# Optimization experiments

Hardware: AMD Instinct MI355X
Metric: run time of the kernel (lower is better)

## Reference

```python
import jax, jax.numpy as jnp
import numpy as np
from jax import lax

K, HE, HD = 4, 96, 192  # kernel_size, hidden_enc, hidden_dec (HD == 2*HE required by z -> decoder hidden)

def _conv1d(x, W, b):
    y = lax.conv_general_dilated(x, W, (1,), 'VALID', dimension_numbers=('NCH', 'OIH', 'NCH'))
    return y + b[None, :, None]

def _maxpool1d(x, k):
    return lax.reduce_window(x, -jnp.inf, lax.max, (1, 1, k), (1, 1, k), 'VALID')

def _gru_scan(x, h0, Wi, Wh, bi, bh, emit):
    # x: (B, S, D); standard PyTorch GRU cell math
    xw = jnp.einsum('bsd,gd->sbg', x, Wi) + bi  # (S, B, 3H)
    def step(h, xw_t):
        xr, xz, xn = jnp.split(xw_t, 3, axis=-1)
        hr, hz, hn = jnp.split(h @ Wh.T + bh, 3, axis=-1)
        r = jax.nn.sigmoid(xr + hr)
        zg = jax.nn.sigmoid(xz + hz)
        n = jnp.tanh(xn + r * hn)
        h_new = (1.0 - zg) * n + zg * h
        return h_new, (h_new if emit else None)
    return lax.scan(step, h0, xw)

def _bigru(x, Wif, Whf, bif, bhf, Wib, Whb, bib, bhb, H):
    h0 = jnp.zeros((x.shape[0], H), x.dtype)
    _, of = _gru_scan(x, h0, Wif, Whf, bif, bhf, True)           # (S, B, H)
    _, ob = _gru_scan(x[:, ::-1], h0, Wib, Whb, bib, bhb, True)  # reverse direction
    return jnp.swapaxes(jnp.concatenate([of, ob[::-1]], axis=-1), 0, 1)  # (B, S, 2H)

def _forward(input, W_c1, b_c1, W_c2, b_c2, Wi_muf, Wh_muf, bi_muf, bh_muf, Wi_mub, Wh_mub, bi_mub, bh_mub, Wi_sgf, Wh_sgf, bi_sgf, bh_sgf, Wi_sgb, Wh_sgb, bi_sgb, bh_sgb, Wi_d, Wh_d, bi_d, bh_d, Wl, bl):
    T = input.shape[1]  # input: (B, T, T); input_dim == seq_len == T
    # Encoder: NodeConv (conv -> relu -> maxpool -> conv -> relu); dropout=0 -> identity
    h = jax.nn.relu(_conv1d(input, W_c1, b_c1))
    h = _maxpool1d(h, K)
    h = jax.nn.relu(_conv1d(h, W_c2, b_c2))  # (B, C, F)
    om = _bigru(h, Wi_muf, Wh_muf, bi_muf, bh_muf, Wi_mub, Wh_mub, bi_mub, bh_mub, HE)
    mu = jnp.concatenate([om[:, -1, :HE], om[:, 0, HE:]], axis=1)
    og = _bigru(h, Wi_sgf, Wh_sgf, bi_sgf, bh_sgf, Wi_sgb, Wh_sgb, bi_sgb, bh_sgb, HE)
    logvar = jnp.concatenate([og[:, -1, :HE], og[:, 0, HE:]], axis=1)
    eps = jax.random.normal(jax.random.key(42), mu.shape, mu.dtype)  # fixed-eps reparameterize
    z = mu + eps * jnp.exp(0.5 * logvar)  # (B, HD)
    # Decoder: leave-one-out per-timestep GRU recompute; hidden carried across outer steps
    base = jnp.arange(T - 1)
    def outer(h_c, i):
        idx = base + (base >= i).astype(base.dtype)  # indices skipping position i
        seq = jnp.take(input, idx, axis=1)           # (B, T-1, T)
        h_new, _ = _gru_scan(seq, h_c, Wi_d, Wh_d, bi_d, bh_d, False)
        return h_new, h_new @ Wl.T + bl
    _, outs = lax.scan(outer, z, jnp.arange(T))
    return jnp.swapaxes(outs, 0, 1), mu, logvar  # (B, T, T), (B, HD), (B, HD)

def setup_inputs():
    keys = iter(jax.random.split(jax.random.key(0), 40))
    def w(*shape):
        return jax.random.normal(next(keys), shape, jnp.float32) * 0.1
    B, D, C, F = 16, 96, 64, 20  # F = ((96-4+1)//4) - 4 + 1
    inp = {"input": jax.random.normal(next(keys), (B, D, D), jnp.float32)}
    inp["W_c1"], inp["b_c1"] = w(C, D, K), jnp.zeros((C,), jnp.float32)
    inp["W_c2"], inp["b_c2"] = w(C, C, K), jnp.zeros((C,), jnp.float32)
    for nm in ["muf", "mub", "sgf", "sgb"]:
        inp["Wi_" + nm] = w(3 * HE, F)
        inp["Wh_" + nm] = w(3 * HE, HE)
        inp["bi_" + nm] = jnp.zeros((3 * HE,), jnp.float32)
        inp["bh_" + nm] = jnp.zeros((3 * HE,), jnp.float32)
    inp["Wi_d"], inp["Wh_d"] = w(3 * HD, D), w(3 * HD, HD)
    inp["bi_d"], inp["bh_d"] = jnp.zeros((3 * HD,), jnp.float32), jnp.zeros((3 * HD,), jnp.float32)
    inp["Wl"], inp["bl"] = w(D, HD), jnp.zeros((D,), jnp.float32)
    return inp

def reference(input, W_c1, b_c1, W_c2, b_c2, Wi_muf, Wh_muf, bi_muf, bh_muf, Wi_mub, Wh_mub, bi_mub, bh_mub, Wi_sgf, Wh_sgf, bi_sgf, bh_sgf, Wi_sgb, Wh_sgb, bi_sgb, bh_sgb, Wi_d, Wh_d, bi_d, bh_d, Wl, bl):
    return _forward(input, W_c1, b_c1, W_c2, b_c2, Wi_muf, Wh_muf, bi_muf, bh_muf, Wi_mub, Wh_mub, bi_mub, bh_mub, Wi_sgf, Wh_sgf, bi_sgf, bh_sgf, Wi_sgb, Wh_sgb, bi_sgb, bh_sgb, Wi_d, Wh_d, bi_d, bh_d, Wl, bl)
```

## Files before the change

kernel.cpp:

```cpp
#include <hip/hip_runtime.h>
#include <math.h>
#include <stdint.h>


namespace {

constexpr int B  = 16;
constexpr int T  = 96;
constexpr int C  = 64;
constexpr int L1 = 93;
constexpr int LP = 23;
constexpr int F  = 20;
constexpr int HE = 96;
constexpr int GE = 288;
constexpr int HD = 192;
constexpr int GD = 576;
constexpr int SD = 95;

constexpr int WS_HENC = 0;
constexpr int WS_Z    = WS_HENC + B * C * F;
constexpr int WS_XW   = WS_Z + B * HD;
constexpr int WS_WHH  = WS_XW + B * T * GD;

constexpr int OUT_MU = B * T * T;
constexpr int OUT_LV = OUT_MU + B * HD;

typedef _Float16 half8 __attribute__((ext_vector_type(8)));
typedef float f32x4  __attribute__((ext_vector_type(4)));

constexpr float LOG2E  = 1.4426950408889634f;
constexpr float LOG2E2 = 2.8853900817779268f;

__device__ __forceinline__ float sigmf(float x) { return 1.0f / (1.0f + expf(-x)); }

__device__ __forceinline__ float fsig(float v) {
  float u = __builtin_amdgcn_exp2f(v * -LOG2E);
  return __builtin_amdgcn_rcpf(1.0f + u);
}
__device__ __forceinline__ float ftanh(float v) {
  float u = __builtin_amdgcn_exp2f(v * LOG2E2);
  return fmaf(-2.0f, __builtin_amdgcn_rcpf(1.0f + u), 1.0f);
}

__global__ __launch_bounds__(256) void enc_conv(
    const float* __restrict__ input, const float* __restrict__ Wc1,
    const float* __restrict__ bc1, const float* __restrict__ Wc2,
    const float* __restrict__ bc2, float* __restrict__ h_enc) {
  __shared__ float xin[T * T];
  __shared__ float y1[C * L1];
  const int b = blockIdx.x;
  for (int i = threadIdx.x; i < T * T; i += 256) xin[i] = input[b * T * T + i];
  __syncthreads();
  for (int idx = threadIdx.x; idx < C * L1; idx += 256) {
    const int o = idx / L1, t = idx - o * L1;
    const float* w = Wc1 + o * (T * 4);
    float acc = bc1[o];
#pragma unroll 8
    for (int i = 0; i < T; ++i) {
      float4 wv = *reinterpret_cast<const float4*>(w + i * 4);
      const float* xp = xin + i * T + t;
      acc = fmaf(wv.x, xp[0], acc);
      acc = fmaf(wv.y, xp[1], acc);
      acc = fmaf(wv.z, xp[2], acc);
      acc = fmaf(wv.w, xp[3], acc);
    }
    y1[idx] = fmaxf(acc, 0.0f);
  }
  __syncthreads();
  float* pl = xin;
  for (int idx = threadIdx.x; idx < C * LP; idx += 256) {
    const int o = idx / LP, t = idx - o * LP;
    const float* yp = y1 + o * L1 + 4 * t;
    pl[idx] = fmaxf(fmaxf(yp[0], yp[1]), fmaxf(yp[2], yp[3]));
  }
  __syncthreads();
  for (int idx = threadIdx.x; idx < C * F; idx += 256) {
    const int o = idx / F, t = idx - o * F;
    const float* w = Wc2 + o * (C * 4);
    float acc = bc2[o];
#pragma unroll 8
    for (int i = 0; i < C; ++i) {
      float4 wv = *reinterpret_cast<const float4*>(w + i * 4);
      const float* xp = pl + i * LP + t;
      acc = fmaf(wv.x, xp[0], acc);
      acc = fmaf(wv.y, xp[1], acc);
      acc = fmaf(wv.z, xp[2], acc);
      acc = fmaf(wv.w, xp[3], acc);
    }
    h_enc[b * (C * F) + idx] = fmaxf(acc, 0.0f);
  }
}

__global__ __launch_bounds__(320) void enc_gru(
    const float* __restrict__ h_enc,
    const float* __restrict__ Wi0, const float* __restrict__ Wh0,
    const float* __restrict__ bi0, const float* __restrict__ bh0,
    const float* __restrict__ Wi1, const float* __restrict__ Wh1,
    const float* __restrict__ bi1, const float* __restrict__ bh1,
    const float* __restrict__ Wi2, const float* __restrict__ Wh2,
    const float* __restrict__ bi2, const float* __restrict__ bh2,
    const float* __restrict__ Wi3, const float* __restrict__ Wh3,
    const float* __restrict__ bi3, const float* __restrict__ bh3,
    float* __restrict__ out) {
  const int chain = blockIdx.x >> 4;
  const int b = blockIdx.x & 15;
  const float *Wi, *Wh, *bi, *bh;
  if (chain == 0)      { Wi = Wi0; Wh = Wh0; bi = bi0; bh = bh0; }
  else if (chain == 1) { Wi = Wi1; Wh = Wh1; bi = bi1; bh = bh1; }
  else if (chain == 2) { Wi = Wi2; Wh = Wh2; bi = bi2; bh = bh2; }
  else                 { Wi = Wi3; Wh = Wh3; bi = bi3; bh = bh3; }
  const bool fwd = (chain & 1) == 0;
  const int off = ((chain >> 1) ? OUT_LV : OUT_MU) + b * HD + (fwd ? 0 : HE);

  __shared__ float xall[C * F];
  __shared__ float h[HE];
  __shared__ float gx[GE], ghs[GE];

  const int tid = threadIdx.x;
  for (int i = tid; i < C * F; i += 320) xall[i] = h_enc[b * (C * F) + i];
  if (tid < HE) h[tid] = 0.0f;

  float wi[F], wh[HE], big = 0.0f, bhg = 0.0f;
  if (tid < GE) {
#pragma unroll
    for (int d = 0; d < F; ++d) wi[d] = Wi[tid * F + d];
#pragma unroll
    for (int k = 0; k < HE; ++k) wh[k] = Wh[tid * HE + k];
    big = bi[tid];
    bhg = bh[tid];
  }
  __syncthreads();

  for (int s = 0; s < C; ++s) {
    const int se = fwd ? s : (C - 1 - s);
    if (tid < GE) {
      const float* xr = xall + se * F;
      float ax = big, ah = bhg;
#pragma unroll
      for (int d = 0; d < F; ++d) ax = fmaf(wi[d], xr[d], ax);
#pragma unroll
      for (int k = 0; k < HE; ++k) ah = fmaf(wh[k], h[k], ah);
      gx[tid] = ax;
      ghs[tid] = ah;
    }
    __syncthreads();
    if (tid < HE) {
      const float r  = sigmf(gx[tid] + ghs[tid]);
      const float zg = sigmf(gx[HE + tid] + ghs[HE + tid]);
      const float n  = tanhf(fmaf(r, ghs[2 * HE + tid], gx[2 * HE + tid]));
      h[tid] = fmaf(zg, h[tid] - n, n);
    }
    __syncthreads();
  }
  if (tid < HE) out[off + tid] = h[tid];
}

__device__ __forceinline__ uint32_t rotl32(uint32_t v, int d) {
  return (v << d) | (v >> (32 - d));
}

__device__ __forceinline__ float erfinv32(float x) {
  float w = -log1pf(-x * x);
  float p;
  if (w < 5.0f) {
    w -= 2.5f;
    p = 2.81022636e-08f;
    p = fmaf(p, w, 3.43273939e-07f);
    p = fmaf(p, w, -3.5233877e-06f);
    p = fmaf(p, w, -4.39150654e-06f);
    p = fmaf(p, w, 0.00021858087f);
    p = fmaf(p, w, -0.00125372503f);
    p = fmaf(p, w, -0.00417768164f);
    p = fmaf(p, w, 0.246640727f);
    p = fmaf(p, w, 1.50140941f);
  } else {
    w = sqrtf(w) - 3.0f;
    p = -0.000200214257f;
    p = fmaf(p, w, 0.000100950558f);
    p = fmaf(p, w, 0.00134934322f);
    p = fmaf(p, w, -0.00367342844f);
    p = fmaf(p, w, 0.00573950773f);
    p = fmaf(p, w, -0.0076224613f);
    p = fmaf(p, w, 0.00943887047f);
    p = fmaf(p, w, 1.00167406f);
    p = fmaf(p, w, 2.83297682f);
  }
  return p * x;
}

__global__ __launch_bounds__(256) void z_kernel(const float* __restrict__ dout,
                                                float* __restrict__ z) {
  const int p = blockIdx.x * 256 + threadIdx.x;
  if (p >= 1536) return;
  const uint32_t ks0 = 0u, ks1 = 42u;
  const uint32_t ks2 = 0x1BD11BDAu ^ ks0 ^ ks1;
  uint32_t x0 = (uint32_t)p + ks0;
  uint32_t x1 = (uint32_t)(p + 1536) + ks1;
  x0 += x1; x1 = rotl32(x1, 13) ^ x0;
  x0 += x1; x1 = rotl32(x1, 15) ^ x0;
  x0 += x1; x1 = rotl32(x1, 26) ^ x0;
  x0 += x1; x1 = rotl32(x1, 6)  ^ x0;
  x0 += ks1; x1 += ks2 + 1u;
  x0 += x1; x1 = rotl32(x1, 17) ^ x0;
  x0 += x1; x1 = rotl32(x1, 29) ^ x0;
  x0 += x1; x1 = rotl32(x1, 16) ^ x0;
  x0 += x1; x1 = rotl32(x1, 24) ^ x0;
  x0 += ks2; x1 += ks0 + 2u;
  x0 += x1; x1 = rotl32(x1, 13) ^ x0;
  x0 += x1; x1 = rotl32(x1, 15) ^ x0;
  x0 += x1; x1 = rotl32(x1, 26) ^ x0;
  x0 += x1; x1 = rotl32(x1, 6)  ^ x0;
  x0 += ks0; x1 += ks1 + 3u;
  x0 += x1; x1 = rotl32(x1, 17) ^ x0;
  x0 += x1; x1 = rotl32(x1, 29) ^ x0;
  x0 += x1; x1 = rotl32(x1, 16) ^ x0;
  x0 += x1; x1 = rotl32(x1, 24) ^ x0;
  x0 += ks1; x1 += ks2 + 4u;
  x0 += x1; x1 = rotl32(x1, 13) ^ x0;
  x0 += x1; x1 = rotl32(x1, 15) ^ x0;
  x0 += x1; x1 = rotl32(x1, 26) ^ x0;
  x0 += x1; x1 = rotl32(x1, 6)  ^ x0;
  x0 += ks2; x1 += ks0 + 5u;

  const float* mu = dout + OUT_MU;
  const float* lv = dout + OUT_LV;
  const float lo = -0.99999994f;
#pragma unroll
  for (int half = 0; half < 2; ++half) {
    const uint32_t bits = half ? x1 : x0;
    const int e = half ? (p + 1536) : p;
    const float f = __builtin_bit_cast(float, (bits >> 9) | 0x3F800000u) - 1.0f;
    const float u = fmaxf(lo, fmaf(f, 2.0f, lo));
    const float eps = 1.41421356f * erfinv32(u);
    z[e] = fmaf(eps, expf(0.5f * lv[e]), mu[e]);
  }
}

__global__ __launch_bounds__(192) void dec_xw(const float* __restrict__ input,
                                              const float* __restrict__ Wi,
                                              const float* __restrict__ bi,
                                              const float* __restrict__ bh,
                                              float* __restrict__ XW) {
  const int br = blockIdx.x;
  __shared__ float xrow[T];
  if (threadIdx.x < T) xrow[threadIdx.x] = input[br * T + threadIdx.x];
  __syncthreads();
  for (int g = threadIdx.x; g < GD; g += 192) {
    const float* w = Wi + g * T;
    float acc = bi[g] + (g < 2 * HD ? bh[g] : 0.0f);
#pragma unroll 8
    for (int d = 0; d < T; ++d) acc = fmaf(w[d], xrow[d], acc);
    XW[br * GD + g] = acc;
  }
}

__global__ __launch_bounds__(256) void wh_to_f16(const float* __restrict__ w,
                                                 _Float16* __restrict__ o) {
  const int i = blockIdx.x * 256 + threadIdx.x;
  if (i < GD * HD) o[i] = (_Float16)w[i];
}

__global__ __launch_bounds__(768) void decoder(
    const float* __restrict__ XW, const _Float16* __restrict__ WhH,
    const float* __restrict__ bh, const float* __restrict__ z,
    const float* __restrict__ Wl, const float* __restrict__ bl,
    float* __restrict__ dout) {
  const int b = blockIdx.x;
  const int tid = threadIdx.x;
  const int lane = tid & 63;
  const int w = tid >> 6;
  const int col = lane & 15;
  const int g4 = lane >> 4;
  const int hidx = 16 * w + col;

  __shared__ alignas(16) _Float16 hb[2][HD];
  __shared__ alignas(16) float hf[HD];

  half8 bR[6], bZ[6], bN[6];
#pragma unroll
  for (int kk = 0; kk < 6; ++kk) {
    const int ko = 32 * kk + 8 * g4;
    bR[kk] = *reinterpret_cast<const half8*>(WhH + hidx * HD + ko);
    bZ[kk] = *reinterpret_cast<const half8*>(WhH + (HD + hidx) * HD + ko);
    bN[kk] = *reinterpret_cast<const half8*>(WhH + (2 * HD + hidx) * HD + ko);
  }
  const float bhn = bh[2 * HD + hidx];

  float hold = z[b * HD + hidx];
  if (g4 == 0) hb[0][hidx] = (_Float16)hold;
  __syncthreads();

  const f32x4 kZero = {0.0f, 0.0f, 0.0f, 0.0f};
  int cur = 0;
  const float* xwb = XW + b * T * GD;

  for (int i = 0; i < T; ++i) {
    for (int s = 0; s < SD; ++s) {
      const int rr = s + (s >= i ? 1 : 0);
      const float* xwrow = xwb + rr * GD;
      const float xr = xwrow[hidx];
      const float xz = xwrow[HD + hidx];
      const float xn = xwrow[2 * HD + hidx];

      half8 a[6];
#pragma unroll
      for (int kk = 0; kk < 6; ++kk)
        a[kk] = *reinterpret_cast<const half8*>(&hb[cur][32 * kk + 8 * g4]);

      f32x4 aR = __builtin_amdgcn_mfma_f32_16x16x32_f16(a[0], bR[0], kZero, 0, 0, 0);
      f32x4 aZ = __builtin_amdgcn_mfma_f32_16x16x32_f16(a[0], bZ[0], kZero, 0, 0, 0);
      f32x4 aN = __builtin_amdgcn_mfma_f32_16x16x32_f16(a[0], bN[0], kZero, 0, 0, 0);
#pragma unroll
      for (int kk = 1; kk < 6; ++kk) {
        aR = __builtin_amdgcn_mfma_f32_16x16x32_f16(a[kk], bR[kk], aR, 0, 0, 0);
        aZ = __builtin_amdgcn_mfma_f32_16x16x32_f16(a[kk], bZ[kk], aZ, 0, 0, 0);
        aN = __builtin_amdgcn_mfma_f32_16x16x32_f16(a[kk], bN[kk], aN, 0, 0, 0);
      }
      const float r  = fsig(xr + aR[0]);
      const float zg = fsig(xz + aZ[0]);
      const float n  = ftanh(fmaf(r, aN[0] + bhn, xn));
      hold = fmaf(zg, hold - n, n);

      if (g4 == 0) {
        hb[cur ^ 1][hidx] = (_Float16)hold;
        if (s == SD - 1) hf[hidx] = hold;
      }
      __syncthreads();
      cur ^= 1;
    }
    if (tid < T) {
      const float4* wl = reinterpret_cast<const float4*>(Wl + tid * HD);
      const float4* hv = reinterpret_cast<const float4*>(hf);
      float a0 = bl[tid], a1 = 0.f, a2 = 0.f, a3 = 0.f;
#pragma unroll
      for (int k = 0; k < HD / 4; k += 4) {
        float4 w0 = wl[k], h0 = hv[k];
        float4 w1 = wl[k + 1], h1 = hv[k + 1];
        float4 w2 = wl[k + 2], h2 = hv[k + 2];
        float4 w3 = wl[k + 3], h3 = hv[k + 3];
        a0 = fmaf(w0.x, h0.x, fmaf(w0.y, h0.y, fmaf(w0.z, h0.z, fmaf(w0.w, h0.w, a0))));
        a1 = fmaf(w1.x, h1.x, fmaf(w1.y, h1.y, fmaf(w1.z, h1.z, fmaf(w1.w, h1.w, a1))));
        a2 = fmaf(w2.x, h2.x, fmaf(w2.y, h2.y, fmaf(w2.z, h2.z, fmaf(w2.w, h2.w, a2))));
        a3 = fmaf(w3.x, h3.x, fmaf(w3.y, h3.y, fmaf(w3.z, h3.z, fmaf(w3.w, h3.w, a3))));
      }
      dout[(b * T + i) * T + tid] = (a0 + a1) + (a2 + a3);
    }
  }
}

}

extern "C" void kernel_launch(void* const* d_in, const int* in_sizes, int n_in,
                              void* d_out, int out_size, void* d_ws,
                              size_t ws_size, hipStream_t stream) {
  const float* input  = (const float*)d_in[0];
  const float* Wc1    = (const float*)d_in[1];
  const float* bc1    = (const float*)d_in[2];
  const float* Wc2    = (const float*)d_in[3];
  const float* bc2    = (const float*)d_in[4];
  const float* Wi_muf = (const float*)d_in[5];
  const float* Wh_muf = (const float*)d_in[6];
  const float* bi_muf = (const float*)d_in[7];
  const float* bh_muf = (const float*)d_in[8];
  const float* Wi_mub = (const float*)d_in[9];
  const float* Wh_mub = (const float*)d_in[10];
  const float* bi_mub = (const float*)d_in[11];
  const float* bh_mub = (const float*)d_in[12];
  const float* Wi_sgf = (const float*)d_in[13];
  const float* Wh_sgf = (const float*)d_in[14];
  const float* bi_sgf = (const float*)d_in[15];
  const float* bh_sgf = (const float*)d_in[16];
  const float* Wi_sgb = (const float*)d_in[17];
  const float* Wh_sgb = (const float*)d_in[18];
  const float* bi_sgb = (const float*)d_in[19];
  const float* bh_sgb = (const float*)d_in[20];
  const float* Wi_d   = (const float*)d_in[21];
  const float* Wh_d   = (const float*)d_in[22];
  const float* bi_d   = (const float*)d_in[23];
  const float* bh_d   = (const float*)d_in[24];
  const float* Wl     = (const float*)d_in[25];
  const float* bl     = (const float*)d_in[26];

  float* ws = (float*)d_ws;
  float* h_enc = ws + WS_HENC;
  float* zbuf  = ws + WS_Z;
  float* XW    = ws + WS_XW;
  _Float16* WhH = (_Float16*)(ws + WS_WHH);
  float* out = (float*)d_out;

  enc_conv<<<B, 256, 0, stream>>>(input, Wc1, bc1, Wc2, bc2, h_enc);
  enc_gru<<<64, 320, 0, stream>>>(h_enc, Wi_muf, Wh_muf, bi_muf, bh_muf,
                                  Wi_mub, Wh_mub, bi_mub, bh_mub,
                                  Wi_sgf, Wh_sgf, bi_sgf, bh_sgf,
                                  Wi_sgb, Wh_sgb, bi_sgb, bh_sgb, out);
  z_kernel<<<6, 256, 0, stream>>>(out, zbuf);
  dec_xw<<<B * T, 192, 0, stream>>>(input, Wi_d, bi_d, bh_d, XW);
  wh_to_f16<<<(GD * HD + 255) / 256, 256, 0, stream>>>(Wh_d, WhH);
  decoder<<<B, 768, 0, stream>>>(XW, WhH, bh_d, zbuf, Wl, bl, out);
}
```

Before: 6.453 ms.

## Batch all decoder sequences into the MFMA M dimension in one block

The decoder now runs as a single 768-thread block that puts all 16 batch rows into the M dimension of each 16x16x32 MFMA. Previously each of 16 blocks used only row 0 of its MFMA output, so most of every tile was wasted. Each lane now handles four batch rows per step: it loads their XW gate inputs and does the gate math for each. LOG2E factors are folded into XW, the f16 recurrent weights and the bias, which removes the scaling multiplies from the sigmoid and tanh paths, and the shared hidden buffers are padded to a stride of 200. The cost is more per-step work on the serial critical path inside one CU, while the other CUs sit idle.

```diff
diff --git a/kernel.cpp b/kernel.cpp
--- a/kernel.cpp
+++ b/kernel.cpp
@@ -16,6 +16,7 @@
 constexpr int HD = 192;
 constexpr int GD = 576;
 constexpr int SD = 95;
+constexpr int HS = 200;
 
 constexpr int WS_HENC = 0;
 constexpr int WS_Z    = WS_HENC + B * C * F;
@@ -33,13 +34,11 @@
 
 __device__ __forceinline__ float sigmf(float x) { return 1.0f / (1.0f + expf(-x)); }
 
-__device__ __forceinline__ float fsig(float v) {
-  float u = __builtin_amdgcn_exp2f(v * -LOG2E);
-  return __builtin_amdgcn_rcpf(1.0f + u);
-}
-__device__ __forceinline__ float ftanh(float v) {
-  float u = __builtin_amdgcn_exp2f(v * LOG2E2);
-  return fmaf(-2.0f, __builtin_amdgcn_rcpf(1.0f + u), 1.0f);
+__device__ __forceinline__ float fsig2(float xp) {
+  return __builtin_amdgcn_rcpf(1.0f + __builtin_amdgcn_exp2f(-xp));
+}
+__device__ __forceinline__ float ftanh2(float vp) {
+  return fmaf(-2.0f, __builtin_amdgcn_rcpf(1.0f + __builtin_amdgcn_exp2f(vp)), 1.0f);
 }
 
 __global__ __launch_bounds__(256) void enc_conv(
@@ -250,31 +249,32 @@
     float acc = bi[g] + (g < 2 * HD ? bh[g] : 0.0f);
 #pragma unroll 8
     for (int d = 0; d < T; ++d) acc = fmaf(w[d], xrow[d], acc);
-    XW[br * GD + g] = acc;
+    XW[br * GD + g] = acc * (g < 2 * HD ? LOG2E : LOG2E2);
   }
 }
 
 __global__ __launch_bounds__(256) void wh_to_f16(const float* __restrict__ w,
                                                  _Float16* __restrict__ o) {
   const int i = blockIdx.x * 256 + threadIdx.x;
-  if (i < GD * HD) o[i] = (_Float16)w[i];
-}
-
-__global__ __launch_bounds__(768) void decoder(
+  if (i < GD * HD)
+    o[i] = (_Float16)(w[i] * (i < 2 * HD * HD ? LOG2E : LOG2E2));
+}
+
+__global__ __launch_bounds__(768, 3) void decoder(
     const float* __restrict__ XW, const _Float16* __restrict__ WhH,
     const float* __restrict__ bh, const float* __restrict__ z,
     const float* __restrict__ Wl, const float* __restrict__ bl,
     float* __restrict__ dout) {
-  const int b = blockIdx.x;
   const int tid = threadIdx.x;
   const int lane = tid & 63;
   const int w = tid >> 6;
   const int col = lane & 15;
   const int g4 = lane >> 4;
   const int hidx = 16 * w + col;
-
-  __shared__ alignas(16) _Float16 hb[2][HD];
-  __shared__ alignas(16) float hf[HD];
+  const int mb = 4 * g4;
+
+  __shared__ alignas(16) _Float16 hb[2][B][HS];
+  __shared__ alignas(16) float hf[B][HS];
 
   half8 bR[6], bZ[6], bN[6];
 #pragma unroll
@@ -284,28 +284,42 @@
     bZ[kk] = *reinterpret_cast<const half8*>(WhH + (HD + hidx) * HD + ko);
     bN[kk] = *reinterpret_cast<const half8*>(WhH + (2 * HD + hidx) * HD + ko);
   }
-  const float bhn = bh[2 * HD + hidx];
-
-  float hold = z[b * HD + hidx];
-  if (g4 == 0) hb[0][hidx] = (_Float16)hold;
+  const float bhn = bh[2 * HD + hidx] * LOG2E2;
+
+  float hold[4];
+#pragma unroll
+  for (int j = 0; j < 4; ++j) hold[j] = z[(mb + j) * HD + hidx];
+  for (int idx = tid; idx < B * HD; idx += 768) {
+    const int bb = idx / HD, k = idx - bb * HD;
+    hb[0][bb][k] = (_Float16)z[idx];
+  }
   __syncthreads();
 
   const f32x4 kZero = {0.0f, 0.0f, 0.0f, 0.0f};
+  const _Float16* ha0 = &hb[0][col][8 * g4];
+  constexpr int BUF = B * HS;
   int cur = 0;
-  const float* xwb = XW + b * T * GD;
+
+  const int tq = tid % 96;
+  const int b0 = tid / 96;
 
   for (int i = 0; i < T; ++i) {
     for (int s = 0; s < SD; ++s) {
       const int rr = s + (s >= i ? 1 : 0);
-      const float* xwrow = xwb + rr * GD;
-      const float xr = xwrow[hidx];
-      const float xz = xwrow[HD + hidx];
-      const float xn = xwrow[2 * HD + hidx];
-
+      float xr[4], xz[4], xn[4];
+#pragma unroll
+      for (int j = 0; j < 4; ++j) {
+        const float* xwrow = XW + ((mb + j) * T + rr) * GD + hidx;
+        xr[j] = xwrow[0];
+        xz[j] = xwrow[HD];
+        xn[j] = xwrow[2 * HD];
+      }
+
+      const _Float16* hp = ha0 + cur;
       half8 a[6];
 #pragma unroll
       for (int kk = 0; kk < 6; ++kk)
-        a[kk] = *reinterpret_cast<const half8*>(&hb[cur][32 * kk + 8 * g4]);
+        a[kk] = *reinterpret_cast<const half8*>(hp + 32 * kk);
 
       f32x4 aR = __builtin_amdgcn_mfma_f32_16x16x32_f16(a[0], bR[0], kZero, 0, 0, 0);
       f32x4 aZ = __builtin_amdgcn_mfma_f32_16x16x32_f16(a[0], bZ[0], kZero, 0, 0, 0);
@@ -316,22 +330,30 @@
         aZ = __builtin_amdgcn_mfma_f32_16x16x32_f16(a[kk], bZ[kk], aZ, 0, 0, 0);
         aN = __builtin_amdgcn_mfma_f32_16x16x32_f16(a[kk], bN[kk], aN, 0, 0, 0);
       }
-      const float r  = fsig(xr + aR[0]);
-      const float zg = fsig(xz + aZ[0]);
-      const float n  = ftanh(fmaf(r, aN[0] + bhn, xn));
-      hold = fmaf(zg, hold - n, n);
-
-      if (g4 == 0) {
-        hb[cur ^ 1][hidx] = (_Float16)hold;
-        if (s == SD - 1) hf[hidx] = hold;
+
+      const int nxt = cur ^ BUF;
+      _Float16* hw = &hb[0][0][0] + nxt + (mb * HS + hidx);
+#pragma unroll
+      for (int j = 0; j < 4; ++j) {
+        const float r  = fsig2(xr[j] + aR[j]);
+        const float zg = fsig2(xz[j] + aZ[j]);
+        const float n  = ftanh2(fmaf(r, aN[j] + bhn, xn[j]));
+        hold[j] = fmaf(zg, hold[j] - n, n);
+        hw[j * HS] = (_Float16)hold[j];
+      }
+      if (s == SD - 1) {
+#pragma unroll
+        for (int j = 0; j < 4; ++j) hf[mb + j][hidx] = hold[j];
       }
       __syncthreads();
-      cur ^= 1;
-    }
-    if (tid < T) {
-      const float4* wl = reinterpret_cast<const float4*>(Wl + tid * HD);
-      const float4* hv = reinterpret_cast<const float4*>(hf);
-      float a0 = bl[tid], a1 = 0.f, a2 = 0.f, a3 = 0.f;
+      cur = nxt;
+    }
+#pragma unroll
+    for (int rep = 0; rep < 2; ++rep) {
+      const int bb = b0 + 8 * rep;
+      const float4* wl = reinterpret_cast<const float4*>(Wl + tq * HD);
+      const float4* hv = reinterpret_cast<const float4*>(&hf[bb][0]);
+      float a0 = bl[tq], a1 = 0.f, a2 = 0.f, a3 = 0.f;
 #pragma unroll
       for (int k = 0; k < HD / 4; k += 4) {
         float4 w0 = wl[k], h0 = hv[k];
@@ -343,7 +365,7 @@
         a2 = fmaf(w2.x, h2.x, fmaf(w2.y, h2.y, fmaf(w2.z, h2.z, fmaf(w2.w, h2.w, a2))));
         a3 = fmaf(w3.x, h3.x, fmaf(w3.y, h3.y, fmaf(w3.z, h3.z, fmaf(w3.w, h3.w, a3))));
       }
-      dout[(b * T + i) * T + tid] = (a0 + a1) + (a2 + a3);
+      dout[(bb * T + i) * T + tq] = (a0 + a1) + (a2 + a3);
     }
   }
 }
@@ -396,5 +418,5 @@
   z_kernel<<<6, 256, 0, stream>>>(out, zbuf);
   dec_xw<<<B * T, 192, 0, stream>>>(input, Wi_d, bi_d, bh_d, XW);
   wh_to_f16<<<(GD * HD + 255) / 256, 256, 0, stream>>>(Wh_d, WhH);
-  decoder<<<B, 768, 0, stream>>>(XW, WhH, bh_d, zbuf, Wl, bl, out);
-}
+  decoder<<<1, 768, 0, stream>>>(XW, WhH, bh_d, zbuf, Wl, bl, out);
+}
```

Measured after the change: 12.03 ms (median of 6 runs). 86.4% more time.
